# Performance work log

Hardware: AMD Instinct MI355X
Metric: run time of the kernel (lower is better)

## Reference

```python
import jax, jax.numpy as jnp
import numpy as np
import math

BS, S, DIM, H = 2, 2048, 1024, 16
DH = DIM // H


def setup_inputs() -> dict:
    key = jax.random.key(0)
    ks = jax.random.split(key, 11)
    std = 1.0 / math.sqrt(DIM)
    inp = {
        "query": jax.random.normal(ks[0], (BS, S, DIM), jnp.float32),
        "key_": jax.random.normal(ks[1], (BS, S, DIM), jnp.float32),
        "value": jax.random.normal(ks[2], (BS, S, DIM), jnp.float32),
        "mask": jnp.ones((BS, S), jnp.int32),
        "q_w": jax.random.normal(ks[3], (DIM, DIM), jnp.float32) * std,
        "q_b": jnp.zeros((DIM,), jnp.float32),
        "k_w": jax.random.normal(ks[4], (DIM, DIM), jnp.float32) * std,
        "k_b": jnp.zeros((DIM,), jnp.float32),
        "v_w": jax.random.normal(ks[5], (DIM, DIM), jnp.float32) * std,
        "v_b": jnp.zeros((DIM,), jnp.float32),
        "o_w": jax.random.normal(ks[6], (DIM, DIM), jnp.float32) * std,
        "o_b": jnp.zeros((DIM,), jnp.float32),
    }
    return inp


def _shape(x):
    # (bs, s, dim) -> (bs, h, s, dh)
    return x.reshape(BS, -1, H, DH).transpose(0, 2, 1, 3)


def reference(query, key_, value, mask, q_w, q_b, k_w, k_b, v_w, v_b, o_w, o_b):
    # linear projections (torch Linear: x @ W.T + b)
    q = _shape(query @ q_w.T + q_b) / math.sqrt(DH)
    k = _shape(key_ @ k_w.T + k_b)
    v = _shape(value @ v_w.T + v_b)
    # scores: (bs, h, s, s)
    scores = jnp.einsum("bhqd,bhkd->bhqk", q, k)
    pad = (mask == 0)[:, None, None, :]  # (bs,1,1,k_len)
    scores = jnp.where(pad, -jnp.inf, scores)
    weights = jax.nn.softmax(scores, axis=-1)
    context = jnp.einsum("bhqk,bhkd->bhqd", weights, v)
    context = context.transpose(0, 2, 1, 3).reshape(BS, -1, DIM)
    return context @ o_w.T + o_b
```

## Files before the change

### kernel.cpp

```cpp
#include <hip/hip_runtime.h>
#include <hip/hip_bf16.h>

#define BSZ 2
#define SEQ 2048
#define DIMN 1024
#define NH 16
#define DH 64
#define LOG2E 1.4426950408889634f

typedef unsigned short ushort_t;
typedef __attribute__((ext_vector_type(8))) short short8;
typedef __attribute__((ext_vector_type(4))) float float4v;

__device__ __forceinline__ ushort_t f2bf(float f) {
    union { float f; unsigned int u; } c; c.f = f;
    return (ushort_t)((c.u + 0x8000u) >> 16);
}
__device__ __forceinline__ unsigned int pkbf(float a, float b) {
    __hip_bfloat162 h = __float22bfloat162_rn(make_float2(a, b));
    unsigned int u; __builtin_memcpy(&u, &h, 4); return u;
}

__global__ __launch_bounds__(256) void cvt_w(
    const float* __restrict__ w0, const float* __restrict__ w1,
    const float* __restrict__ w2, const float* __restrict__ w3,
    ushort_t* __restrict__ o0, ushort_t* __restrict__ o1,
    ushort_t* __restrict__ o2, ushort_t* __restrict__ o3)
{
    const float* s; ushort_t* d;
    switch (blockIdx.y) {
        case 0: s = w0; d = o0; break;
        case 1: s = w1; d = o1; break;
        case 2: s = w2; d = o2; break;
        default: s = w3; d = o3; break;
    }
    int i = (blockIdx.x * 256 + threadIdx.x) * 4;
    float4v v = *(const float4v*)(s + i);
    uint2 o; o.x = pkbf(v[0], v[1]); o.y = pkbf(v[2], v[3]);
    *(uint2*)(d + i) = o;
}

__global__ __launch_bounds__(256) void gemm_qkv(
    const float* __restrict__ xq, const float* __restrict__ xk, const float* __restrict__ xv,
    const ushort_t* __restrict__ Wq, const ushort_t* __restrict__ Wk, const ushort_t* __restrict__ Wv,
    const float* __restrict__ qb, const float* __restrict__ kb, const float* __restrict__ vb,
    ushort_t* __restrict__ Qp, ushort_t* __restrict__ Kp, ushort_t* __restrict__ VpT)
{
    __shared__ ushort_t As[128 * 72];
    __shared__ ushort_t Bs[128 * 72];
    const int tid  = threadIdx.x;
    const int lane = tid & 63;
    const int w    = tid >> 6;
    const int wm   = w >> 1, wn = w & 1;
    const int quad = lane >> 4;
    const int l16  = lane & 15;
    const int mBase = blockIdx.y * 128;
    const int nGlob = blockIdx.x * 128;
    const int z     = nGlob >> 10;
    const int nBase = nGlob & 1023;
    const float*    A    = (z == 0) ? xq : (z == 1) ? xk : xv;
    const ushort_t* W    = (z == 0) ? Wq : (z == 1) ? Wk : Wv;
    const float*    bias = (z == 0) ? qb : (z == 1) ? kb : vb;

    float4v acc[4][4];
    const float4v z4 = {0.f, 0.f, 0.f, 0.f};
#pragma unroll
    for (int i = 0; i < 4; ++i)
#pragma unroll
        for (int j = 0; j < 4; ++j) acc[i][j] = z4;

    for (int k0 = 0; k0 < 1024; k0 += 64) {
        float4v a[4][2];
        short8  wb[4];
#pragma unroll
        for (int it = 0; it < 4; ++it) {
            int c = it * 256 + tid, row = c >> 3, col = (c & 7) * 8;
            const float* g = A + (size_t)(mBase + row) * 1024 + k0 + col;
            a[it][0] = *(const float4v*)g;
            a[it][1] = *(const float4v*)(g + 4);
            wb[it] = *(const short8*)(W + (size_t)(nBase + row) * 1024 + k0 + col);
        }
        __syncthreads();
#pragma unroll
        for (int it = 0; it < 4; ++it) {
            int c = it * 256 + tid, row = c >> 3, col = (c & 7) * 8;
            uint4 ua;
            ua.x = pkbf(a[it][0][0], a[it][0][1]); ua.y = pkbf(a[it][0][2], a[it][0][3]);
            ua.z = pkbf(a[it][1][0], a[it][1][1]); ua.w = pkbf(a[it][1][2], a[it][1][3]);
            *(uint4*)&As[row * 72 + col] = ua;
            *(short8*)&Bs[row * 72 + col] = wb[it];
        }
        __syncthreads();

#pragma unroll
        for (int ksub = 0; ksub < 2; ++ksub) {
            short8 af[4], bf[4];
#pragma unroll
            for (int mt = 0; mt < 4; ++mt)
                af[mt] = *(const short8*)&As[(wm * 64 + mt * 16 + l16) * 72 + ksub * 32 + quad * 8];
#pragma unroll
            for (int nt = 0; nt < 4; ++nt)
                bf[nt] = *(const short8*)&Bs[(wn * 64 + nt * 16 + l16) * 72 + ksub * 32 + quad * 8];
#pragma unroll
            for (int mt = 0; mt < 4; ++mt)
#pragma unroll
                for (int nt = 0; nt < 4; ++nt)
                    acc[mt][nt] = __builtin_amdgcn_mfma_f32_16x16x32_bf16(af[mt], bf[nt], acc[mt][nt], 0, 0, 0);
        }
    }

    const float scale = (z == 0) ? 0.125f * LOG2E : 1.0f;
    if (z < 2) {
        ushort_t* C = (z == 0) ? Qp : Kp;
#pragma unroll
        for (int mt = 0; mt < 4; ++mt)
#pragma unroll
            for (int nt = 0; nt < 4; ++nt) {
                int colg = nBase + wn * 64 + nt * 16 + l16;
                float bv = bias[colg];
#pragma unroll
                for (int r = 0; r < 4; ++r) {
                    int rowg = mBase + wm * 64 + mt * 16 + quad * 4 + r;
                    C[(size_t)rowg * 1024 + colg] = f2bf((acc[mt][nt][r] + bv) * scale);
                }
            }
    } else {
#pragma unroll
        for (int mt = 0; mt < 4; ++mt)
#pragma unroll
            for (int nt = 0; nt < 4; ++nt) {
                int n = nBase + wn * 64 + nt * 16 + l16;
                int hh = n >> 6, d = n & 63;
                float bv = bias[n];
                int rowg = mBase + wm * 64 + mt * 16 + quad * 4;
                int b = rowg >> 11, s = rowg & 2047;
                uint2 pk;
                pk.x = pkbf(acc[mt][nt][0] + bv, acc[mt][nt][1] + bv);
                pk.y = pkbf(acc[mt][nt][2] + bv, acc[mt][nt][3] + bv);
                *(uint2*)&VpT[(((size_t)(b * 16 + hh) * 64 + d) << 11) + s] = pk;
            }
    }
}

__global__ __launch_bounds__(256) void gemm_o(
    const ushort_t* __restrict__ A, const ushort_t* __restrict__ W,
    const float* __restrict__ bias, float* __restrict__ C)
{
    __shared__ ushort_t As[128 * 72];
    __shared__ ushort_t Bs[64 * 72];
    const int tid  = threadIdx.x;
    const int lane = tid & 63;
    const int w    = tid >> 6;
    const int wm   = w & 1, wn = w >> 1;
    const int quad = lane >> 4;
    const int l16  = lane & 15;
    const int mBase = blockIdx.y * 128;
    const int nBase = blockIdx.x * 64;

    float4v acc[4][2];
    const float4v z4 = {0.f, 0.f, 0.f, 0.f};
#pragma unroll
    for (int mt = 0; mt < 4; ++mt)
#pragma unroll
        for (int nt = 0; nt < 2; ++nt) acc[mt][nt] = z4;

    for (int k0 = 0; k0 < 1024; k0 += 64) {
        short8 ab[4], wb[2];
#pragma unroll
        for (int it = 0; it < 4; ++it) {
            int c = it * 256 + tid, row = c >> 3, col = (c & 7) * 8;
            ab[it] = *(const short8*)(A + (size_t)(mBase + row) * 1024 + k0 + col);
        }
#pragma unroll
        for (int it = 0; it < 2; ++it) {
            int c = it * 256 + tid, row = c >> 3, col = (c & 7) * 8;
            wb[it] = *(const short8*)(W + (size_t)(nBase + row) * 1024 + k0 + col);
        }
        __syncthreads();
#pragma unroll
        for (int it = 0; it < 4; ++it) {
            int c = it * 256 + tid, row = c >> 3, col = (c & 7) * 8;
            *(short8*)&As[row * 72 + col] = ab[it];
        }
#pragma unroll
        for (int it = 0; it < 2; ++it) {
            int c = it * 256 + tid, row = c >> 3, col = (c & 7) * 8;
            *(short8*)&Bs[row * 72 + col] = wb[it];
        }
        __syncthreads();

#pragma unroll
        for (int ksub = 0; ksub < 2; ++ksub) {
            short8 af[4], bf[2];
#pragma unroll
            for (int mt = 0; mt < 4; ++mt)
                af[mt] = *(const short8*)&As[(wm * 64 + mt * 16 + l16) * 72 + ksub * 32 + quad * 8];
#pragma unroll
            for (int nt = 0; nt < 2; ++nt)
                bf[nt] = *(const short8*)&Bs[(wn * 32 + nt * 16 + l16) * 72 + ksub * 32 + quad * 8];
#pragma unroll
            for (int mt = 0; mt < 4; ++mt)
#pragma unroll
                for (int nt = 0; nt < 2; ++nt)
                    acc[mt][nt] = __builtin_amdgcn_mfma_f32_16x16x32_bf16(af[mt], bf[nt], acc[mt][nt], 0, 0, 0);
        }
    }

#pragma unroll
    for (int mt = 0; mt < 4; ++mt)
#pragma unroll
        for (int nt = 0; nt < 2; ++nt) {
            int colg = nBase + wn * 32 + nt * 16 + l16;
            float bv = bias[colg];
#pragma unroll
            for (int r = 0; r < 4; ++r) {
                int rowg = mBase + wm * 64 + mt * 16 + quad * 4 + r;
                C[(size_t)rowg * 1024 + colg] = acc[mt][nt][r] + bv;
            }
        }
}

__global__ __launch_bounds__(512) void attn_kernel(
    const ushort_t* __restrict__ Qp, const ushort_t* __restrict__ Kp,
    const ushort_t* __restrict__ VpT, const int* __restrict__ mask,
    ushort_t* __restrict__ Cp)
{
    __shared__ ushort_t QPs[128 * 72];
    __shared__ ushort_t Ks[64 * 72];
    __shared__ ushort_t Vt[64 * 72];

    const int tid  = threadIdx.x;
    const int lane = tid & 63;
    const int w    = tid >> 6;
    const int quad = lane >> 4;
    const int l16  = lane & 15;
    const int b    = blockIdx.x >> 4;
    const int h    = blockIdx.x & 15;
    const int q0   = blockIdx.y * 128;

    {
        short8 qreg[2];
#pragma unroll
        for (int it = 0; it < 2; ++it) {
            int c = it * 512 + tid, row = c >> 3, col = (c & 7) * 8;
            qreg[it] = *(const short8*)(Qp + (size_t)(b * SEQ + q0 + row) * DIMN + h * DH + col);
        }
#pragma unroll
        for (int it = 0; it < 2; ++it) {
            int c = it * 512 + tid, row = c >> 3, col = (c & 7) * 8;
            *(short8*)&QPs[row * 72 + col] = qreg[it];
        }
    }
    __syncthreads();
    short8 bq[2];
#pragma unroll
    for (int ks = 0; ks < 2; ++ks)
        bq[ks] = *(const short8*)&QPs[(w * 16 + l16) * 72 + ks * 32 + quad * 8];

    const float4v z4 = {0.f, 0.f, 0.f, 0.f};
    float4v Oacc[4];
#pragma unroll
    for (int vt = 0; vt < 4; ++vt) Oacc[vt] = z4;
    float4v Lacc = z4;
    float mrow = -3e38f;

    short8 ones;
#pragma unroll
    for (int j = 0; j < 8; ++j) ones[j] = (short)0x3F80;

    const ushort_t* Vbase = VpT + ((size_t)(b * 16 + h) * 64) * 2048;
    const int srow = tid >> 3, scol = (tid & 7) * 8;

    for (int kt0 = 0; kt0 < SEQ; kt0 += 64) {
        short8 kreg = *(const short8*)(Kp + (size_t)(b * SEQ + kt0 + srow) * DIMN + h * DH + scol);
        short8 vreg = *(const short8*)(Vbase + (size_t)srow * 2048 + kt0 + scol);
        int4 mv4[4];
#pragma unroll
        for (int kt = 0; kt < 4; ++kt)
            mv4[kt] = *(const int4*)(mask + b * SEQ + kt0 + kt * 16 + quad * 4);

        __syncthreads();
        *(short8*)&Ks[srow * 72 + scol] = kreg;
        *(short8*)&Vt[srow * 72 + scol] = vreg;
        __syncthreads();

        float4v Sv[4];
#pragma unroll
        for (int kt = 0; kt < 4; ++kt) Sv[kt] = z4;
#pragma unroll
        for (int ks = 0; ks < 2; ++ks)
#pragma unroll
            for (int kt = 0; kt < 4; ++kt) {
                short8 ak = *(const short8*)&Ks[(kt * 16 + l16) * 72 + ks * 32 + quad * 8];
                Sv[kt] = __builtin_amdgcn_mfma_f32_16x16x32_bf16(ak, bq[ks], Sv[kt], 0, 0, 0);
            }

        int allm = (mv4[0].x & mv4[0].y & mv4[0].z & mv4[0].w) &
                   (mv4[1].x & mv4[1].y & mv4[1].z & mv4[1].w) &
                   (mv4[2].x & mv4[2].y & mv4[2].z & mv4[2].w) &
                   (mv4[3].x & mv4[3].y & mv4[3].z & mv4[3].w);
        if (__any(allm == 0)) {
#pragma unroll
            for (int kt = 0; kt < 4; ++kt) {
                int4 mv = mv4[kt];
#pragma unroll
                for (int r = 0; r < 4; ++r) {
                    int m = (r == 0) ? mv.x : (r == 1) ? mv.y : (r == 2) ? mv.z : mv.w;
                    Sv[kt][r] += (m == 0) ? -1e30f : 0.0f;
                }
            }
        }

        float mx = Sv[0][0];
#pragma unroll
        for (int kt = 0; kt < 4; ++kt)
#pragma unroll
            for (int r = 0; r < 4; ++r) mx = fmaxf(mx, Sv[kt][r]);
        mx = fmaxf(mx, __shfl_xor(mx, 16));
        mx = fmaxf(mx, __shfl_xor(mx, 32));
        float mn = fmaxf(mrow, mx);
        float alpha = exp2f(mrow - mn);
        mrow = mn;
#pragma unroll
        for (int kt = 0; kt < 4; ++kt)
#pragma unroll
            for (int r = 0; r < 4; ++r) Sv[kt][r] = exp2f(Sv[kt][r] - mn);
#pragma unroll
        for (int vt = 0; vt < 4; ++vt) Oacc[vt] *= alpha;
        Lacc *= alpha;

#pragma unroll
        for (int kt = 0; kt < 4; ++kt) {
            uint2 pk;
            pk.x = pkbf(Sv[kt][0], Sv[kt][1]);
            pk.y = pkbf(Sv[kt][2], Sv[kt][3]);
            *(uint2*)&QPs[(w * 16 + l16) * 72 + kt * 16 + quad * 4] = pk;
        }

#pragma unroll
        for (int ks = 0; ks < 2; ++ks) {
            short8 bp = *(const short8*)&QPs[(w * 16 + l16) * 72 + ks * 32 + quad * 8];
            Lacc = __builtin_amdgcn_mfma_f32_16x16x32_bf16(ones, bp, Lacc, 0, 0, 0);
#pragma unroll
            for (int vt = 0; vt < 4; ++vt) {
                short8 av = *(const short8*)&Vt[(vt * 16 + l16) * 72 + ks * 32 + quad * 8];
                Oacc[vt] = __builtin_amdgcn_mfma_f32_16x16x32_bf16(av, bp, Oacc[vt], 0, 0, 0);
            }
        }
    }

    float inv = 1.0f / Lacc[0];
    int row = q0 + w * 16 + l16;
#pragma unroll
    for (int vt = 0; vt < 4; ++vt) {
        uint2 pk;
        pk.x = pkbf(Oacc[vt][0] * inv, Oacc[vt][1] * inv);
        pk.y = pkbf(Oacc[vt][2] * inv, Oacc[vt][3] * inv);
        *(uint2*)&Cp[(size_t)(b * SEQ + row) * DIMN + h * DH + vt * 16 + quad * 4] = pk;
    }
}

extern "C" void kernel_launch(void* const* d_in, const int* in_sizes, int n_in,
                              void* d_out, int out_size, void* d_ws, size_t ws_size,
                              hipStream_t stream) {
    const float* x_q = (const float*)d_in[0];
    const float* x_k = (const float*)d_in[1];
    const float* x_v = (const float*)d_in[2];
    const int*   msk = (const int*)d_in[3];
    const float* q_w = (const float*)d_in[4];
    const float* q_b = (const float*)d_in[5];
    const float* k_w = (const float*)d_in[6];
    const float* k_b = (const float*)d_in[7];
    const float* v_w = (const float*)d_in[8];
    const float* v_b = (const float*)d_in[9];
    const float* o_w = (const float*)d_in[10];
    const float* o_b = (const float*)d_in[11];
    float* out = (float*)d_out;

    const size_t NEL = (size_t)BSZ * SEQ * DIMN;
    const size_t WEL = (size_t)DIMN * DIMN;
    ushort_t* Qp  = (ushort_t*)d_ws;
    ushort_t* Kp  = Qp + NEL;
    ushort_t* VpT = Kp + NEL;
    ushort_t* Wq  = VpT + NEL;
    ushort_t* Wk  = Wq + WEL;
    ushort_t* Wv  = Wk + WEL;
    ushort_t* Wo  = Wv + WEL;
    ushort_t* Cp  = Qp;

    cvt_w<<<dim3(WEL / 1024, 4), 256, 0, stream>>>(q_w, k_w, v_w, o_w, Wq, Wk, Wv, Wo);
    gemm_qkv<<<dim3(24, 32), 256, 0, stream>>>(x_q, x_k, x_v, Wq, Wk, Wv,
                                               q_b, k_b, v_b, Qp, Kp, VpT);
    attn_kernel<<<dim3(BSZ * NH, SEQ / 128), 512, 0, stream>>>(Qp, Kp, VpT, msk, Cp);
    gemm_o<<<dim3(16, 32), 256, 0, stream>>>(Cp, Wo, o_b, out);
}
```

Measured before the change: 266.6 us.

## Double-buffer K/V tiles, hoist mask check, lazy softmax rescale in attention

The attention loop now keeps two LDS buffers for K and V. The next tile is stored while the current one is computed, and the tile after that is prefetched into registers, which cuts the loop to one barrier per iteration. A single up-front pass over the mask decides whether any key is padded, so per-tile mask loads are skipped when none are. The online-softmax rescale is skipped unless the new max exceeds the running max by more than 8 (log2 units), and MFMA sections are given raised wave priority. The lazy rescale lets exponentials grow up to 2^8 before normalisation, which slightly changes the rounding of the bf16 P values.

New measurement: 264.1 us. Within noise of the previous version (-0.9%).

```diff
diff --git a/kernel.cpp b/kernel.cpp
--- a/kernel.cpp
+++ b/kernel.cpp
@@ -226,8 +226,9 @@
     ushort_t* __restrict__ Cp)
 {
     __shared__ ushort_t QPs[128 * 72];
-    __shared__ ushort_t Ks[64 * 72];
-    __shared__ ushort_t Vt[64 * 72];
+    __shared__ ushort_t Ks[2][64 * 72];
+    __shared__ ushort_t Vt[2][64 * 72];
+    __shared__ int s_mok[8];
 
     const int tid  = threadIdx.x;
     const int lane = tid & 63;
@@ -238,20 +239,41 @@
     const int h    = blockIdx.x & 15;
     const int q0   = blockIdx.y * 128;
 
+    const int srow = tid >> 3, scol = (tid & 7) * 8;
+    const ushort_t* Vbase = VpT + ((size_t)(b * 16 + h) * 64) * 2048;
+    const ushort_t* Kbase = Kp + (size_t)b * SEQ * DIMN + h * DH;
+
     {
-        short8 qreg[2];
-#pragma unroll
-        for (int it = 0; it < 2; ++it) {
-            int c = it * 512 + tid, row = c >> 3, col = (c & 7) * 8;
-            qreg[it] = *(const short8*)(Qp + (size_t)(b * SEQ + q0 + row) * DIMN + h * DH + col);
-        }
-#pragma unroll
-        for (int it = 0; it < 2; ++it) {
-            int c = it * 512 + tid, row = c >> 3, col = (c & 7) * 8;
-            *(short8*)&QPs[row * 72 + col] = qreg[it];
-        }
-    }
+        int m0 = mask[b * SEQ + tid];
+        int m1 = mask[b * SEQ + 512 + tid];
+        int m2 = mask[b * SEQ + 1024 + tid];
+        int m3 = mask[b * SEQ + 1536 + tid];
+        int ok = __all((m0 != 0) & (m1 != 0) & (m2 != 0) & (m3 != 0));
+        if (lane == 0) s_mok[w] = ok;
+    }
+
+    short8 qreg[2];
+#pragma unroll
+    for (int it = 0; it < 2; ++it) {
+        int c = it * 512 + tid, row = c >> 3, col = (c & 7) * 8;
+        qreg[it] = *(const short8*)(Qp + (size_t)(b * SEQ + q0 + row) * DIMN + h * DH + col);
+    }
+    short8 kreg = *(const short8*)(Kbase + (size_t)srow * DIMN + scol);
+    short8 vreg = *(const short8*)(Vbase + (size_t)srow * 2048 + scol);
+#pragma unroll
+    for (int it = 0; it < 2; ++it) {
+        int c = it * 512 + tid, row = c >> 3, col = (c & 7) * 8;
+        *(short8*)&QPs[row * 72 + col] = qreg[it];
+    }
+    *(short8*)&Ks[0][srow * 72 + scol] = kreg;
+    *(short8*)&Vt[0][srow * 72 + scol] = vreg;
+    kreg = *(const short8*)(Kbase + (size_t)(64 + srow) * DIMN + scol);
+    vreg = *(const short8*)(Vbase + (size_t)srow * 2048 + 64 + scol);
     __syncthreads();
+
+    const int mall = s_mok[0] & s_mok[1] & s_mok[2] & s_mok[3]
+                   & s_mok[4] & s_mok[5] & s_mok[6] & s_mok[7];
+
     short8 bq[2];
 #pragma unroll
     for (int ks = 0; ks < 2; ++ks)
@@ -268,38 +290,38 @@
 #pragma unroll
     for (int j = 0; j < 8; ++j) ones[j] = (short)0x3F80;
 
-    const ushort_t* Vbase = VpT + ((size_t)(b * 16 + h) * 64) * 2048;
-    const int srow = tid >> 3, scol = (tid & 7) * 8;
-
-    for (int kt0 = 0; kt0 < SEQ; kt0 += 64) {
-        short8 kreg = *(const short8*)(Kp + (size_t)(b * SEQ + kt0 + srow) * DIMN + h * DH + scol);
-        short8 vreg = *(const short8*)(Vbase + (size_t)srow * 2048 + kt0 + scol);
-        int4 mv4[4];
-#pragma unroll
-        for (int kt = 0; kt < 4; ++kt)
-            mv4[kt] = *(const int4*)(mask + b * SEQ + kt0 + kt * 16 + quad * 4);
-
-        __syncthreads();
-        *(short8*)&Ks[srow * 72 + scol] = kreg;
-        *(short8*)&Vt[srow * 72 + scol] = vreg;
-        __syncthreads();
+    for (int it = 0; it < SEQ / 64; ++it) {
+        const int bsel = it & 1;
+        const int kt0  = it * 64;
+
+        if (it + 1 < SEQ / 64) {
+            *(short8*)&Ks[bsel ^ 1][srow * 72 + scol] = kreg;
+            *(short8*)&Vt[bsel ^ 1][srow * 72 + scol] = vreg;
+        }
+        if (it + 2 < SEQ / 64) {
+            int kn = kt0 + 128;
+            kreg = *(const short8*)(Kbase + (size_t)(kn + srow) * DIMN + scol);
+            vreg = *(const short8*)(Vbase + (size_t)srow * 2048 + kn + scol);
+        }
 
         float4v Sv[4];
 #pragma unroll
         for (int kt = 0; kt < 4; ++kt) Sv[kt] = z4;
+        __builtin_amdgcn_s_setprio(1);
 #pragma unroll
         for (int ks = 0; ks < 2; ++ks)
 #pragma unroll
             for (int kt = 0; kt < 4; ++kt) {
-                short8 ak = *(const short8*)&Ks[(kt * 16 + l16) * 72 + ks * 32 + quad * 8];
+                short8 ak = *(const short8*)&Ks[bsel][(kt * 16 + l16) * 72 + ks * 32 + quad * 8];
                 Sv[kt] = __builtin_amdgcn_mfma_f32_16x16x32_bf16(ak, bq[ks], Sv[kt], 0, 0, 0);
             }
-
-        int allm = (mv4[0].x & mv4[0].y & mv4[0].z & mv4[0].w) &
-                   (mv4[1].x & mv4[1].y & mv4[1].z & mv4[1].w) &
-                   (mv4[2].x & mv4[2].y & mv4[2].z & mv4[2].w) &
-                   (mv4[3].x & mv4[3].y & mv4[3].z & mv4[3].w);
-        if (__any(allm == 0)) {
+        __builtin_amdgcn_s_setprio(0);
+
+        if (!mall) {
+            int4 mv4[4];
+#pragma unroll
+            for (int kt = 0; kt < 4; ++kt)
+                mv4[kt] = *(const int4*)(mask + b * SEQ + kt0 + kt * 16 + quad * 4);
 #pragma unroll
             for (int kt = 0; kt < 4; ++kt) {
                 int4 mv = mv4[kt];
@@ -318,16 +340,18 @@
             for (int r = 0; r < 4; ++r) mx = fmaxf(mx, Sv[kt][r]);
         mx = fmaxf(mx, __shfl_xor(mx, 16));
         mx = fmaxf(mx, __shfl_xor(mx, 32));
-        float mn = fmaxf(mrow, mx);
-        float alpha = exp2f(mrow - mn);
-        mrow = mn;
+        if (!__all(mx - mrow <= 8.0f)) {
+            float mn = fmaxf(mrow, mx);
+            float alpha = exp2f(mrow - mn);
+            mrow = mn;
+#pragma unroll
+            for (int vt = 0; vt < 4; ++vt) Oacc[vt] *= alpha;
+            Lacc *= alpha;
+        }
 #pragma unroll
         for (int kt = 0; kt < 4; ++kt)
 #pragma unroll
-            for (int r = 0; r < 4; ++r) Sv[kt][r] = exp2f(Sv[kt][r] - mn);
-#pragma unroll
-        for (int vt = 0; vt < 4; ++vt) Oacc[vt] *= alpha;
-        Lacc *= alpha;
+            for (int r = 0; r < 4; ++r) Sv[kt][r] = exp2f(Sv[kt][r] - mrow);
 
 #pragma unroll
         for (int kt = 0; kt < 4; ++kt) {
@@ -337,16 +361,20 @@
             *(uint2*)&QPs[(w * 16 + l16) * 72 + kt * 16 + quad * 4] = pk;
         }
 
+        __builtin_amdgcn_s_setprio(1);
 #pragma unroll
         for (int ks = 0; ks < 2; ++ks) {
             short8 bp = *(const short8*)&QPs[(w * 16 + l16) * 72 + ks * 32 + quad * 8];
             Lacc = __builtin_amdgcn_mfma_f32_16x16x32_bf16(ones, bp, Lacc, 0, 0, 0);
 #pragma unroll
             for (int vt = 0; vt < 4; ++vt) {
-                short8 av = *(const short8*)&Vt[(vt * 16 + l16) * 72 + ks * 32 + quad * 8];
+                short8 av = *(const short8*)&Vt[bsel][(vt * 16 + l16) * 72 + ks * 32 + quad * 8];
                 Oacc[vt] = __builtin_amdgcn_mfma_f32_16x16x32_bf16(av, bp, Oacc[vt], 0, 0, 0);
             }
         }
+        __builtin_amdgcn_s_setprio(0);
+
+        __syncthreads();
     }
 
     float inv = 1.0f / Lacc[0];
```
